# Kernel optimization log

Hardware: AMD Instinct MI355X
Metric: run time of the kernel (lower is better)

## Reference

```python
import jax, jax.numpy as jnp
import numpy as np

DIM = 64
HID = 64      # hidden_dim
BATCH = 16384


def setup_inputs() -> dict:
    key = jax.random.key(0)
    ks = jax.random.split(key, 11)
    s = 0.05
    x = jax.random.normal(ks[0], (BATCH, DIM), dtype=jnp.float32)
    # network 0: Linear(1,H) -> ReLU -> Linear(H,2)
    w0 = jax.random.normal(ks[1], (1, HID), dtype=jnp.float32) * s
    b0 = jax.random.normal(ks[2], (HID,), dtype=jnp.float32) * s
    v0 = jax.random.normal(ks[3], (HID, 2), dtype=jnp.float32) * s
    c0 = jax.random.normal(ks[4], (2,), dtype=jnp.float32) * s
    # networks 1..DIM-1: Linear(i,H) -> ReLU -> Linear(H,H) -> ReLU -> Linear(H,2)
    # first-layer weights padded to full width DIM; columns >= i are masked out in reference().
    W1 = jax.random.normal(ks[5], (DIM - 1, DIM, HID), dtype=jnp.float32) * s
    B1 = jax.random.normal(ks[6], (DIM - 1, HID), dtype=jnp.float32) * s
    W2 = jax.random.normal(ks[7], (DIM - 1, HID, HID), dtype=jnp.float32) * s
    B2 = jax.random.normal(ks[8], (DIM - 1, HID), dtype=jnp.float32) * s
    W3 = jax.random.normal(ks[9], (DIM - 1, HID, 2), dtype=jnp.float32) * s
    B3 = jax.random.normal(ks[10], (DIM - 1, 2), dtype=jnp.float32) * s
    return {"x": x, "w0": w0, "b0": b0, "v0": v0, "c0": c0,
            "W1": W1, "B1": B1, "W2": W2, "B2": B2, "W3": W3, "B3": B3}


def reference(x, w0, b0, v0, c0, W1, B1, W2, B2, W3, B3):
    B, dim = x.shape
    # mask[i, j] = 1 if j < (i+1): network i+1 sees x[:, :i+1] prefix of width i+1... actually width i+1? No:
    # network index k (k = 1..dim-1) sees x[:, :k]. Row i of the stacks corresponds to k = i+1,
    # so valid input columns are j < i+1.
    mask = (jnp.arange(dim)[None, :] <= jnpp_dummy) if False else (jnp.arange(dim)[None, :] < (jnp.arange(1, dim)[:, None]))
    mask = mask.astype(x.dtype)                      # [dim-1, dim]
    W1m = W1 * mask[:, :, None]                      # zero out padded input columns
    h1 = jax.nn.relu(jnp.einsum('bd,idh->bih', x, W1m) + B1)   # [B, dim-1, H]
    h2 = jax.nn.relu(jnp.einsum('bih,ihg->big', h1, W2) + B2)  # [B, dim-1, H]
    out = jnp.einsum('big,igo->bio', h2, W3) + B3               # [B, dim-1, 2]
    # network 0 receives a constant ones input -> output is constant across the batch
    h0 = jax.nn.relu(w0[0] + b0)                     # [H]
    out0 = h0 @ v0 + c0                              # [2]
    out0 = jnp.broadcast_to(out0[None, None, :], (B, 1, 2))
    full = jnp.concatenate([out0, out], axis=1)      # [B, dim, 2]
    scales = jnp.clip(full[..., 0], -5.0, 5.0)
    translations = full[..., 1]
    return scales, translations

jnp_dummy = None
```

## Files before the change

### kernel.cpp

```cpp
#include <hip/hip_runtime.h>
#include <hip/hip_bf16.h>

#define BATCH 16384

typedef __attribute__((ext_vector_type(8))) short short8;
typedef __attribute__((ext_vector_type(4))) short short4v;
typedef __attribute__((ext_vector_type(2))) short sshort2;
typedef __attribute__((ext_vector_type(8))) unsigned short ushort8;
typedef __attribute__((ext_vector_type(4))) unsigned short ushort4v;
typedef __attribute__((ext_vector_type(4))) float float4v;

#define FR_STRIDE  18944u
#define FR_SIZE    (63u * FR_STRIDE)
#define OFF_A2     8192u
#define OFF_A3     16384u
#define OFF_B1     18432u
#define OFF_B2     18688u
#define XBF_SIZE   2097152u
#define FR_ELEMS   1184

__device__ __forceinline__ unsigned int packbf2(float a, float b) {
#if __has_builtin(__builtin_amdgcn_cvt_pk_bf16_f32)
    typedef __attribute__((ext_vector_type(2))) __bf16 bf2_t;
    union { bf2_t h; unsigned int u; } v;
    v.h = __builtin_amdgcn_cvt_pk_bf16_f32(a, b);
    return v.u;
#else
    union { __hip_bfloat162 h; unsigned int u; } v;
    v.h = __float22bfloat162_rn(make_float2(a, b));
    return v.u;
#endif
}
__device__ __forceinline__ unsigned int relu_pk(unsigned int u) {
#if __has_builtin(__builtin_elementwise_max)
    union { sshort2 s; unsigned int w; } v; v.w = u;
    v.s = __builtin_elementwise_max(v.s, (sshort2)0);
    return v.w;
#else
    unsigned int lo = (u & 0x8000u) ? 0u : (u & 0xFFFFu);
    unsigned int hi = (u & 0x80000000u) ? 0u : (u & 0xFFFF0000u);
    return lo | hi;
#endif
}
__device__ __forceinline__ unsigned int cvt_relu(float a, float b) {
    return relu_pk(packbf2(a, b));
}
__device__ __forceinline__ unsigned short f2bf(float a) {
    union { __hip_bfloat16 h; unsigned short u; } v;
    v.h = __float2bfloat16(a);
    return v.u;
}

__device__ __forceinline__ void gl_lds16(const char* gsrc, char* ldst) {
    __builtin_amdgcn_global_load_lds(
        (const __attribute__((address_space(1))) unsigned int*)gsrc,
        (__attribute__((address_space(3))) unsigned int*)ldst,
        16, 0, 0);
}

__global__ __launch_bounds__(256) void setup_kernel(
    const float* __restrict__ x,
    const float* __restrict__ W1,
    const float* __restrict__ W2,
    const float* __restrict__ W3,
    const float* __restrict__ B1,
    const float* __restrict__ B2,
    char* __restrict__ frag,
    char* __restrict__ xbf)
{
    const int b = blockIdx.x;
    const int t = threadIdx.x;

    if (b >= 63) {
        const int idx = (b - 63) * 256 + t;
        const float* xp = x + (size_t)idx * 16;
        char* dst = xbf + (size_t)idx * 32;
        #pragma unroll
        for (int h = 0; h < 2; ++h) {
            float4v f0 = *(const float4v*)(xp + h * 8);
            float4v f1 = *(const float4v*)(xp + h * 8 + 4);
            union { ushort8 s; unsigned int u[4]; } p;
            p.u[0] = packbf2(f0[0], f0[1]);
            p.u[1] = packbf2(f0[2], f0[3]);
            p.u[2] = packbf2(f1[0], f1[1]);
            p.u[3] = packbf2(f1[2], f1[3]);
            *(ushort8*)(dst + h * 16) = p.s;
        }
        return;
    }

    __shared__ float sW1[4096];
    __shared__ float sW2[4096];

    const int kn   = b;
    const int net  = kn + 1;
    const int lane = t & 63;
    const int grp  = t >> 6;
    const int lq   = lane & 15;
    const int quad = lane >> 4;

    {
        const float4v* s1 = (const float4v*)(W1 + kn * 4096);
        const float4v* s2 = (const float4v*)(W2 + kn * 4096);
        #pragma unroll
        for (int i = 0; i < 4; ++i) {
            ((float4v*)sW1)[i * 256 + t] = s1[i * 256 + t];
            ((float4v*)sW2)[i * 256 + t] = s2[i * 256 + t];
        }
    }
    __syncthreads();

    char* base = frag + (size_t)kn * FR_STRIDE;

    {
        const int h = lq + 16 * grp;
        ushort8 a10, a11;
        #pragma unroll
        for (int j = 0; j < 8; ++j) {
            const int d0 = quad * 8 + j;
            const int d1 = d0 + 32;
            a10[j] = (d0 < net) ? f2bf(sW1[d0 * 64 + h]) : (unsigned short)0;
            a11[j] = (d1 < net) ? f2bf(sW1[d1 * 64 + h]) : (unsigned short)0;
        }
        char* dst = base + grp * 2048 + lane * 32;
        *(ushort8*)(dst)      = a10;
        *(ushort8*)(dst + 16) = a11;
    }

    {
        const int g = lq + 16 * grp;
        #pragma unroll
        for (int p = 0; p < 2; ++p) {
            ushort8 v;
            #pragma unroll
            for (int j = 0; j < 8; ++j) {
                const int h = 32 * p + ((j & 4) << 2) + 4 * quad + (j & 3);
                v[j] = f2bf(sW2[h * 64 + g]);
            }
            *(ushort8*)(base + OFF_A2 + p * 4096 + grp * 1024 + lane * 16) = v;
        }
    }

    if (grp < 2) {
        const int p = grp;
        ushort8 v;
        #pragma unroll
        for (int j = 0; j < 8; ++j) {
            const int gg = 32 * p + ((j & 4) << 2) + 4 * quad + (j & 3);
            v[j] = (lq < 2) ? f2bf(W3[kn * 128 + gg * 2 + lq]) : (unsigned short)0;
        }
        *(ushort8*)(base + OFF_A3 + p * 1024 + lane * 16) = v;
    }

    if (t < 64) {
        *(float*)(base + OFF_B1 + t * 4) = B1[kn * 64 + t];
        *(float*)(base + OFF_B2 + t * 4) = B2[kn * 64 + t];
    }
}

template <bool XBF>
__global__ __launch_bounds__(256, 3) void arnet_main4(
    const float* __restrict__ x,
    const char* __restrict__ xbf,
    const char* __restrict__ frag,
    const float* __restrict__ w0, const float* __restrict__ b0,
    const float* __restrict__ v0, const float* __restrict__ c0,
    const float* __restrict__ B3,
    float* __restrict__ out)
{
    const int bi    = blockIdx.x;
    const int chunk = bi & 63;
    const int g     = bi >> 6;
    const int t     = threadIdx.x;

    const int lane = t & 63;
    const int w    = t >> 6;
    const int lq   = lane & 15;
    const int quad = lane >> 4;

    __shared__ __align__(16) char sFrag[2][FR_STRIDE];
    __shared__ float sOut[2][256][5];

    const int rowbase = chunk * 256 + w * 64;

    short8 xf[4][2];
    #pragma unroll
    for (int tm = 0; tm < 4; ++tm) {
        if (XBF) {
            const char* base = xbf + (size_t)(rowbase + 16 * tm + lq) * 128 + quad * 16;
            xf[tm][0] = *(const short8*)(base);
            xf[tm][1] = *(const short8*)(base + 64);
        } else {
            const float* xr = x + (size_t)(rowbase + 16 * tm + lq) * 64 + quad * 8;
            #pragma unroll
            for (int half = 0; half < 2; ++half) {
                float4v f0 = *(const float4v*)(xr + 32 * half);
                float4v f1 = *(const float4v*)(xr + 32 * half + 4);
                union { short8 s; unsigned int u[4]; } p;
                p.u[0] = packbf2(f0[0], f0[1]);
                p.u[1] = packbf2(f0[2], f0[3]);
                p.u[2] = packbf2(f1[0], f1[1]);
                p.u[3] = packbf2(f1[2], f1[3]);
                xf[tm][half] = p.s;
            }
        }
    }

    auto stage = [&](int net_, char* dstb) {
        const char* src = frag + (size_t)(net_ - 1) * FR_STRIDE;
        #pragma unroll
        for (int i = 0; i < 5; ++i) {
            const int e = i * 256 + t;
            if (e < FR_ELEMS)
                gl_lds16(src + e * 16, dstb + e * 16);
        }
    };

    const int first = (g == 0) ? 1 : 0;
    stage(g * 4 + first, sFrag[first & 1]);
    __syncthreads();

    #pragma unroll 1
    for (int idx = 0; idx < 4; ++idx) {
        const int net = g * 4 + idx;

        if (idx + 1 < 4 && idx + 1 > first)
            stage(g * 4 + idx + 1, sFrag[(idx + 1) & 1]);

        if (net == 0) {
            float s = 0.f, tr = 0.f;
            #pragma unroll 8
            for (int j = 0; j < 64; ++j) {
                float h = fmaxf(w0[j] + b0[j], 0.f);
                s  += h * v0[2 * j];
                tr += h * v0[2 * j + 1];
            }
            s += c0[0];
            tr += c0[1];
            s = fminf(fmaxf(s, -5.f), 5.f);
            sOut[0][t][0] = s;
            sOut[1][t][0] = tr;
            __syncthreads();
            continue;
        }

        const int kn = net - 1;
        const char* sf  = sFrag[idx & 1];
        const char* pA1 = sf + lane * 32;
        const char* pA2 = sf + OFF_A2 + lane * 16;
        const char* pA3 = sf + OFF_A3 + lane * 16;
        const float* bB1 = (const float*)(sf + OFF_B1);
        const float* bB2 = (const float*)(sf + OFF_B2);

        float4v acc2[4][4];
        #pragma unroll
        for (int p = 0; p < 2; ++p) {
            unsigned int pk[2][2][4];
            #pragma unroll
            for (int s = 0; s < 2; ++s) {
                const int th = 2 * p + s;
                short8 a10 = *(const short8*)(pA1 + th * 2048);
                short8 a11 = *(const short8*)(pA1 + th * 2048 + 16);
                float4v bias1 = *(const float4v*)(bB1 + quad * 4 + 16 * th);
                #pragma unroll
                for (int tm = 0; tm < 4; ++tm) {
                    float4v acc1;
                    acc1 = __builtin_amdgcn_mfma_f32_16x16x32_bf16(a10, xf[tm][0], bias1, 0, 0, 0);
                    acc1 = __builtin_amdgcn_mfma_f32_16x16x32_bf16(a11, xf[tm][1], acc1, 0, 0, 0);
                    pk[s][0][tm] = cvt_relu(acc1[0], acc1[1]);
                    pk[s][1][tm] = cvt_relu(acc1[2], acc1[3]);
                }
            }
            #pragma unroll
            for (int tg = 0; tg < 4; ++tg) {
                short8 a2 = *(const short8*)(pA2 + p * 4096 + tg * 1024);
                float4v bias2 = *(const float4v*)(bB2 + quad * 4 + 16 * tg);
                #pragma unroll
                for (int tm = 0; tm < 4; ++tm) {
                    union { short8 s8; unsigned int u[4]; } bb;
                    bb.u[0] = pk[0][0][tm]; bb.u[1] = pk[0][1][tm];
                    bb.u[2] = pk[1][0][tm]; bb.u[3] = pk[1][1][tm];
                    acc2[tg][tm] = __builtin_amdgcn_mfma_f32_16x16x32_bf16(
                        a2, bb.s8, (p == 0) ? bias2 : acc2[tg][tm], 0, 0, 0);
                }
            }
        }

        float4v c3v;
        c3v[0] = B3[kn * 2]; c3v[1] = B3[kn * 2 + 1]; c3v[2] = 0.f; c3v[3] = 0.f;
        float4v acc3[4];
        #pragma unroll
        for (int p = 0; p < 2; ++p) {
            short8 a3 = *(const short8*)(pA3 + p * 1024);
            #pragma unroll
            for (int tm = 0; tm < 4; ++tm) {
                union { short8 s8; unsigned int u[4]; } bb;
                bb.u[0] = cvt_relu(acc2[2 * p][tm][0],     acc2[2 * p][tm][1]);
                bb.u[1] = cvt_relu(acc2[2 * p][tm][2],     acc2[2 * p][tm][3]);
                bb.u[2] = cvt_relu(acc2[2 * p + 1][tm][0], acc2[2 * p + 1][tm][1]);
                bb.u[3] = cvt_relu(acc2[2 * p + 1][tm][2], acc2[2 * p + 1][tm][3]);
                acc3[tm] = __builtin_amdgcn_mfma_f32_16x16x32_bf16(
                    a3, bb.s8, (p == 0) ? c3v : acc3[tm], 0, 0, 0);
            }
        }

        if (quad == 0) {
            #pragma unroll
            for (int tm = 0; tm < 4; ++tm) {
                const int lr = w * 64 + 16 * tm + lq;
                sOut[0][lr][idx] = fminf(fmaxf(acc3[tm][0], -5.f), 5.f);
                sOut[1][lr][idx] = acc3[tm][1];
            }
        }
        __syncthreads();
    }

    {
        const int row = t;
        const size_t grow = (size_t)chunk * 256 + row;
        #pragma unroll
        for (int o = 0; o < 2; ++o) {
            float4v v4;
            #pragma unroll
            for (int j = 0; j < 4; ++j) v4[j] = sOut[o][row][j];
            float* dst = out + ((size_t)o * BATCH + grow) * 64 + 4 * g;
            *(float4v*)(dst) = v4;
        }
    }
}

#define WPAD 72
__global__ __launch_bounds__(256) void arnet_fallback(
    const float* __restrict__ x, const float* __restrict__ w0, const float* __restrict__ b0,
    const float* __restrict__ v0, const float* __restrict__ c0,
    const float* __restrict__ W1, const float* __restrict__ B1,
    const float* __restrict__ W2, const float* __restrict__ B2,
    const float* __restrict__ W3, const float* __restrict__ B3,
    float* __restrict__ out)
{
    const int bi = blockIdx.x;
    const int net = bi >> 5;
    const int tile = bi & 31;
    const int t = threadIdx.x;
    if (net == 0) {
        float s = 0.f, tr = 0.f;
        for (int j = 0; j < 64; ++j) {
            float h = fmaxf(w0[j] + b0[j], 0.f);
            s += h * v0[2 * j]; tr += h * v0[2 * j + 1];
        }
        s += c0[0]; tr += c0[1];
        s = fminf(fmaxf(s, -5.f), 5.f);
        const size_t r0 = (size_t)tile * 512;
        out[(r0 + t) * 64] = s; out[(size_t)BATCH * 64 + (r0 + t) * 64] = tr;
        out[(r0 + 256 + t) * 64] = s; out[(size_t)BATCH * 64 + (r0 + 256 + t) * 64] = tr;
        return;
    }
    __shared__ unsigned short sW1T[64 * WPAD];
    __shared__ unsigned short sW2T[64 * WPAD];
    __shared__ unsigned short sW3T[2 * 64];
    __shared__ float sB1[64];
    __shared__ float sB2[64];
    const int kn = net - 1;
    {
        const int hb = (t & 15) * 4, jb = (t >> 4) * 4;
        const float* src1 = W1 + kn * 4096;
        const float* src2 = W2 + kn * 4096;
        float4v a[4], b[4];
        for (int jj = 0; jj < 4; ++jj) {
            a[jj] = *(const float4v*)(src1 + (jb + jj) * 64 + hb);
            if (jb + jj >= net) a[jj] = (float4v)0.f;
            b[jj] = *(const float4v*)(src2 + (jb + jj) * 64 + hb);
        }
        for (int hh = 0; hh < 4; ++hh) {
            ushort4v ra, rb;
            for (int jj = 0; jj < 4; ++jj) { ra[jj] = f2bf(a[jj][hh]); rb[jj] = f2bf(b[jj][hh]); }
            *(ushort4v*)(&sW1T[(hb + hh) * WPAD + jb]) = ra;
            *(ushort4v*)(&sW2T[(hb + hh) * WPAD + jb]) = rb;
        }
    }
    if (t < 64) {
        sW3T[t] = f2bf(W3[kn * 128 + t * 2]);
        sW3T[64 + t] = f2bf(W3[kn * 128 + t * 2 + 1]);
        sB1[t] = B1[kn * 64 + t];
        sB2[t] = B2[kn * 64 + t];
    }
    const float b30 = B3[kn * 2], b31 = B3[kn * 2 + 1];
    __syncthreads();
    const int lane = t & 63, w = t >> 6, lq = lane & 15, quad = lane >> 4;
    for (int pass = 0; pass < 2; ++pass) {
        const int rowbase = tile * 512 + pass * 256 + w * 64;
        short8 xf[4][2];
        for (int tm = 0; tm < 4; ++tm) {
            const float* xr = x + (size_t)(rowbase + 16 * tm + lq) * 64 + quad * 8;
            for (int half = 0; half < 2; ++half) {
                float4v f0 = *(const float4v*)(xr + 32 * half);
                float4v f1 = *(const float4v*)(xr + 32 * half + 4);
                union { short8 s; unsigned int u[4]; } p;
                p.u[0] = packbf2(f0[0], f0[1]); p.u[1] = packbf2(f0[2], f0[3]);
                p.u[2] = packbf2(f1[0], f1[1]); p.u[3] = packbf2(f1[2], f1[3]);
                xf[tm][half] = p.s;
            }
        }
        float4v acc2[4][4];
        for (int tg = 0; tg < 4; ++tg) {
            float4v bias2 = *(const float4v*)(&sB2[quad * 4 + 16 * tg]);
            for (int tm = 0; tm < 4; ++tm) acc2[tg][tm] = bias2;
        }
        for (int th = 0; th < 4; ++th) {
            float4v bias1 = *(const float4v*)(&sB1[quad * 4 + 16 * th]);
            short8 a10 = *(const short8*)(&sW1T[(lq + 16 * th) * WPAD + quad * 8]);
            short8 a11 = *(const short8*)(&sW1T[(lq + 16 * th) * WPAD + quad * 8 + 32]);
            float4v acc1[4];
            for (int tm = 0; tm < 4; ++tm) {
                acc1[tm] = bias1;
                acc1[tm] = __builtin_amdgcn_mfma_f32_16x16x32_bf16(a10, xf[tm][0], acc1[tm], 0, 0, 0);
                acc1[tm] = __builtin_amdgcn_mfma_f32_16x16x32_bf16(a11, xf[tm][1], acc1[tm], 0, 0, 0);
            }
            short4v bf1[4];
            for (int tm = 0; tm < 4; ++tm) {
                union { short4v s; unsigned int u[2]; } pk;
                pk.u[0] = cvt_relu(acc1[tm][0], acc1[tm][1]);
                pk.u[1] = cvt_relu(acc1[tm][2], acc1[tm][3]);
                bf1[tm] = pk.s;
            }
            for (int tg = 0; tg < 4; ++tg) {
                short4v a2 = *(const short4v*)(&sW2T[(lq + 16 * tg) * WPAD + quad * 4 + 16 * th]);
                for (int tm = 0; tm < 4; ++tm)
                    acc2[tg][tm] = __builtin_amdgcn_mfma_f32_16x16x16bf16_1k(a2, bf1[tm], acc2[tg][tm], 0, 0, 0);
            }
        }
        float4v acc3[4];
        for (int tm = 0; tm < 4; ++tm) { acc3[tm][0] = b30; acc3[tm][1] = b31; acc3[tm][2] = 0.f; acc3[tm][3] = 0.f; }
        for (int tg = 0; tg < 4; ++tg) {
            short4v a3 = (short4v)0;
            if (lq < 2) a3 = *(const short4v*)(&sW3T[lq * 64 + quad * 4 + 16 * tg]);
            for (int tm = 0; tm < 4; ++tm) {
                union { short4v s; unsigned int u[2]; } pk;
                pk.u[0] = cvt_relu(acc2[tg][tm][0], acc2[tg][tm][1]);
                pk.u[1] = cvt_relu(acc2[tg][tm][2], acc2[tg][tm][3]);
                acc3[tm] = __builtin_amdgcn_mfma_f32_16x16x16bf16_1k(a3, pk.s, acc3[tm], 0, 0, 0);
            }
        }
        if (quad == 0) {
            for (int tm = 0; tm < 4; ++tm) {
                const size_t r = (size_t)(rowbase + 16 * tm + lq);
                out[r * 64 + net] = fminf(fmaxf(acc3[tm][0], -5.f), 5.f);
                out[(size_t)BATCH * 64 + r * 64 + net] = acc3[tm][1];
            }
        }
    }
}

extern "C" void kernel_launch(void* const* d_in, const int* in_sizes, int n_in,
                              void* d_out, int out_size, void* d_ws, size_t ws_size,
                              hipStream_t stream) {
    const float* x  = (const float*)d_in[0];
    const float* w0 = (const float*)d_in[1];
    const float* b0 = (const float*)d_in[2];
    const float* v0 = (const float*)d_in[3];
    const float* c0 = (const float*)d_in[4];
    const float* W1 = (const float*)d_in[5];
    const float* B1 = (const float*)d_in[6];
    const float* W2 = (const float*)d_in[7];
    const float* B2 = (const float*)d_in[8];
    const float* W3 = (const float*)d_in[9];
    const float* B3 = (const float*)d_in[10];
    float* out = (float*)d_out;
    char* ws = (char*)d_ws;

    const dim3 blk(256);

    if (ws_size >= FR_SIZE + XBF_SIZE) {
        char* xbf = ws + FR_SIZE;
        setup_kernel<<<dim3(63 + 256), blk, 0, stream>>>(x, W1, W2, W3, B1, B2, ws, xbf);
        arnet_main4<true><<<dim3(1024), blk, 0, stream>>>(
            x, xbf, ws, w0, b0, v0, c0, B3, out);
    } else if (ws_size >= FR_SIZE) {
        setup_kernel<<<dim3(63), blk, 0, stream>>>(x, W1, W2, W3, B1, B2, ws, nullptr);
        arnet_main4<false><<<dim3(1024), blk, 0, stream>>>(
            x, nullptr, ws, w0, b0, v0, c0, B3, out);
    } else {
        arnet_fallback<<<dim3(64 * 32), blk, 0, stream>>>(
            x, w0, b0, v0, c0, W1, B1, W2, B2, W3, B3, out);
    }
}
```

Before: 104.0 us.

## Split row tiles into halves, drop LDS output staging, raise occupancy to four

The per-network computation now runs over two halves of the warp's row tiles in a non-unrolled loop, which halves the live accumulator registers (acc2 goes from 4x4 to 4x2). The launch bound is raised from 3 to 4 blocks per SIMD to get more occupancy. The shared sOut staging buffer and its final float4 store are removed, and results are written straight to global memory as scattered scalar stores. This trades coalesced vector writes for lower LDS and register use, and may add uncoalesced write traffic.

```diff
diff --git a/kernel.cpp b/kernel.cpp
--- a/kernel.cpp
+++ b/kernel.cpp
@@ -159,7 +159,7 @@
 }
 
 template <bool XBF>
-__global__ __launch_bounds__(256, 3) void arnet_main4(
+__global__ __launch_bounds__(256, 4) void arnet_main4(
     const float* __restrict__ x,
     const char* __restrict__ xbf,
     const char* __restrict__ frag,
@@ -170,7 +170,8 @@
 {
     const int bi    = blockIdx.x;
     const int chunk = bi & 63;
-    const int g     = bi >> 6;
+    const int gi    = bi >> 6;
+    const int start = gi * 4;
     const int t     = threadIdx.x;
 
     const int lane = t & 63;
@@ -179,7 +180,6 @@
     const int quad = lane >> 4;
 
     __shared__ __align__(16) char sFrag[2][FR_STRIDE];
-    __shared__ float sOut[2][256][5];
 
     const int rowbase = chunk * 256 + w * 64;
 
@@ -216,16 +216,16 @@
         }
     };
 
-    const int first = (g == 0) ? 1 : 0;
-    stage(g * 4 + first, sFrag[first & 1]);
+    const int first = (start == 0) ? 1 : 0;
+    stage(start + first, sFrag[first & 1]);
     __syncthreads();
 
     #pragma unroll 1
     for (int idx = 0; idx < 4; ++idx) {
-        const int net = g * 4 + idx;
+        const int net = start + idx;
 
         if (idx + 1 < 4 && idx + 1 > first)
-            stage(g * 4 + idx + 1, sFrag[(idx + 1) & 1]);
+            stage(start + idx + 1, sFrag[(idx + 1) & 1]);
 
         if (net == 0) {
             float s = 0.f, tr = 0.f;
@@ -238,8 +238,9 @@
             s += c0[0];
             tr += c0[1];
             s = fminf(fmaxf(s, -5.f), 5.f);
-            sOut[0][t][0] = s;
-            sOut[1][t][0] = tr;
+            const size_t grow = (size_t)chunk * 256 + t;
+            out[grow * 64] = s;
+            out[((size_t)BATCH + grow) * 64] = tr;
             __syncthreads();
             continue;
         }
@@ -252,80 +253,73 @@
         const float* bB1 = (const float*)(sf + OFF_B1);
         const float* bB2 = (const float*)(sf + OFF_B2);
 
-        float4v acc2[4][4];
-        #pragma unroll
-        for (int p = 0; p < 2; ++p) {
-            unsigned int pk[2][2][4];
+        const float b30 = B3[kn * 2], b31 = B3[kn * 2 + 1];
+
+        #pragma unroll 1
+        for (int mh = 0; mh < 2; ++mh) {
+            float4v acc2[4][2];
             #pragma unroll
-            for (int s = 0; s < 2; ++s) {
-                const int th = 2 * p + s;
-                short8 a10 = *(const short8*)(pA1 + th * 2048);
-                short8 a11 = *(const short8*)(pA1 + th * 2048 + 16);
-                float4v bias1 = *(const float4v*)(bB1 + quad * 4 + 16 * th);
+            for (int p = 0; p < 2; ++p) {
+                unsigned int pk[2][2][2];
                 #pragma unroll
-                for (int tm = 0; tm < 4; ++tm) {
-                    float4v acc1;
-                    acc1 = __builtin_amdgcn_mfma_f32_16x16x32_bf16(a10, xf[tm][0], bias1, 0, 0, 0);
-                    acc1 = __builtin_amdgcn_mfma_f32_16x16x32_bf16(a11, xf[tm][1], acc1, 0, 0, 0);
-                    pk[s][0][tm] = cvt_relu(acc1[0], acc1[1]);
-                    pk[s][1][tm] = cvt_relu(acc1[2], acc1[3]);
+                for (int s = 0; s < 2; ++s) {
+                    const int th = 2 * p + s;
+                    short8 a10 = *(const short8*)(pA1 + th * 2048);
+                    short8 a11 = *(const short8*)(pA1 + th * 2048 + 16);
+                    float4v bias1 = *(const float4v*)(bB1 + quad * 4 + 16 * th);
+                    #pragma unroll
+                    for (int tm = 0; tm < 2; ++tm) {
+                        float4v acc1;
+                        acc1 = __builtin_amdgcn_mfma_f32_16x16x32_bf16(a10, xf[2 * mh + tm][0], bias1, 0, 0, 0);
+                        acc1 = __builtin_amdgcn_mfma_f32_16x16x32_bf16(a11, xf[2 * mh + tm][1], acc1, 0, 0, 0);
+                        pk[s][0][tm] = cvt_relu(acc1[0], acc1[1]);
+                        pk[s][1][tm] = cvt_relu(acc1[2], acc1[3]);
+                    }
                 }
-            }
+                #pragma unroll
+                for (int tg = 0; tg < 4; ++tg) {
+                    short8 a2 = *(const short8*)(pA2 + p * 4096 + tg * 1024);
+                    float4v bias2 = *(const float4v*)(bB2 + quad * 4 + 16 * tg);
+                    #pragma unroll
+                    for (int tm = 0; tm < 2; ++tm) {
+                        union { short8 s8; unsigned int u[4]; } bb;
+                        bb.u[0] = pk[0][0][tm]; bb.u[1] = pk[0][1][tm];
+                        bb.u[2] = pk[1][0][tm]; bb.u[3] = pk[1][1][tm];
+                        acc2[tg][tm] = __builtin_amdgcn_mfma_f32_16x16x32_bf16(
+                            a2, bb.s8, (p == 0) ? bias2 : acc2[tg][tm], 0, 0, 0);
+                    }
+                }
+            }
+
+            float4v c3v;
+            c3v[0] = b30; c3v[1] = b31; c3v[2] = 0.f; c3v[3] = 0.f;
+            float4v acc3[2];
             #pragma unroll
-            for (int tg = 0; tg < 4; ++tg) {
-                short8 a2 = *(const short8*)(pA2 + p * 4096 + tg * 1024);
-                float4v bias2 = *(const float4v*)(bB2 + quad * 4 + 16 * tg);
+            for (int p = 0; p < 2; ++p) {
+                short8 a3 = *(const short8*)(pA3 + p * 1024);
                 #pragma unroll
-                for (int tm = 0; tm < 4; ++tm) {
+                for (int tm = 0; tm < 2; ++tm) {
                     union { short8 s8; unsigned int u[4]; } bb;
-                    bb.u[0] = pk[0][0][tm]; bb.u[1] = pk[0][1][tm];
-                    bb.u[2] = pk[1][0][tm]; bb.u[3] = pk[1][1][tm];
-                    acc2[tg][tm] = __builtin_amdgcn_mfma_f32_16x16x32_bf16(
-                        a2, bb.s8, (p == 0) ? bias2 : acc2[tg][tm], 0, 0, 0);
+                    bb.u[0] = cvt_relu(acc2[2 * p][tm][0],     acc2[2 * p][tm][1]);
+                    bb.u[1] = cvt_relu(acc2[2 * p][tm][2],     acc2[2 * p][tm][3]);
+                    bb.u[2] = cvt_relu(acc2[2 * p + 1][tm][0], acc2[2 * p + 1][tm][1]);
+                    bb.u[3] = cvt_relu(acc2[2 * p + 1][tm][2], acc2[2 * p + 1][tm][3]);
+                    acc3[tm] = __builtin_amdgcn_mfma_f32_16x16x32_bf16(
+                        a3, bb.s8, (p == 0) ? c3v : acc3[tm], 0, 0, 0);
                 }
             }
-        }
-
-        float4v c3v;
-        c3v[0] = B3[kn * 2]; c3v[1] = B3[kn * 2 + 1]; c3v[2] = 0.f; c3v[3] = 0.f;
-        float4v acc3[4];
-        #pragma unroll
-        for (int p = 0; p < 2; ++p) {
-            short8 a3 = *(const short8*)(pA3 + p * 1024);
-            #pragma unroll
-            for (int tm = 0; tm < 4; ++tm) {
-                union { short8 s8; unsigned int u[4]; } bb;
-                bb.u[0] = cvt_relu(acc2[2 * p][tm][0],     acc2[2 * p][tm][1]);
-                bb.u[1] = cvt_relu(acc2[2 * p][tm][2],     acc2[2 * p][tm][3]);
-                bb.u[2] = cvt_relu(acc2[2 * p + 1][tm][0], acc2[2 * p + 1][tm][1]);
-                bb.u[3] = cvt_relu(acc2[2 * p + 1][tm][2], acc2[2 * p + 1][tm][3]);
-                acc3[tm] = __builtin_amdgcn_mfma_f32_16x16x32_bf16(
-                    a3, bb.s8, (p == 0) ? c3v : acc3[tm], 0, 0, 0);
-            }
-        }
-
-        if (quad == 0) {
-            #pragma unroll
-            for (int tm = 0; tm < 4; ++tm) {
-                const int lr = w * 64 + 16 * tm + lq;
-                sOut[0][lr][idx] = fminf(fmaxf(acc3[tm][0], -5.f), 5.f);
-                sOut[1][lr][idx] = acc3[tm][1];
-            }
-        }
+
+            if (quad == 0) {
+                #pragma unroll
+                for (int tm = 0; tm < 2; ++tm) {
+                    const size_t grow = (size_t)rowbase + 16 * (2 * mh + tm) + lq;
+                    out[grow * 64 + net] = fminf(fmaxf(acc3[tm][0], -5.f), 5.f);
+                    out[((size_t)BATCH + grow) * 64 + net] = acc3[tm][1];
+                }
+            }
+        }
+
         __syncthreads();
-    }
-
-    {
-        const int row = t;
-        const size_t grow = (size_t)chunk * 256 + row;
-        #pragma unroll
-        for (int o = 0; o < 2; ++o) {
-            float4v v4;
-            #pragma unroll
-            for (int j = 0; j < 4; ++j) v4[j] = sOut[o][row][j];
-            float* dst = out + ((size_t)o * BATCH + grow) * 64 + 4 * g;
-            *(float4v*)(dst) = v4;
-        }
     }
 }
 
```

Measured after the change: 198.7 us. 91.0% more time.
